# Kernel optimization log

Measured on AMD Instinct MI355X. Metric: run time of the kernel, lower is better.

Reference implementation:

```python
import jax, jax.numpy as jnp
import numpy as np

HID = 1152
MLP = 4304
NH = 16
HD = HID // NH  # 72
S = 3072
SEGS = 6
EPS = 1e-5


def setup_inputs() -> dict:
    key = jax.random.key(0)
    ks = jax.random.split(key, 16)
    sc = 0.02
    x = jax.random.normal(ks[0], (S, HID), jnp.float32)
    input_row_offsets = (jnp.arange(SEGS + 1, dtype=jnp.int32) * (S // SEGS))
    ang = jax.random.uniform(ks[1], (S, HD // 2), jnp.float32) * 6.2831853
    freqs_cis = jnp.stack([jnp.cos(ang), jnp.sin(ang)], axis=-1)  # [S,36,2]
    return {
        'x': x,
        'input_row_offsets': input_row_offsets,
        'freqs_cis': freqs_cis,
        'ln0_g': jnp.ones((HID,), jnp.float32),
        'ln0_b': jnp.zeros((HID,), jnp.float32),
        'wqkv_w': jax.random.normal(ks[2], (HID, 3 * HID), jnp.float32) * sc,
        'wqkv_b': jnp.zeros((3 * HID,), jnp.float32),
        'wo_w': jax.random.normal(ks[3], (HID, HID), jnp.float32) * sc,
        'wo_b': jnp.zeros((HID,), jnp.float32),
        'ln1_g': jnp.ones((HID,), jnp.float32),
        'ln1_b': jnp.zeros((HID,), jnp.float32),
        'mlp_w1': jax.random.normal(ks[4], (HID, MLP), jnp.float32) * sc,
        'mlp_b1': jnp.zeros((MLP,), jnp.float32),
        'mlp_w2': jax.random.normal(ks[5], (MLP, HID), jnp.float32) * sc,
        'mlp_b2': jnp.zeros((HID,), jnp.float32),
    }


def _layernorm(x, g, b):
    mu = jnp.mean(x, axis=-1, keepdims=True)
    var = jnp.mean(jnp.square(x - mu), axis=-1, keepdims=True)
    return (x - mu) * jax.lax.rsqrt(var + EPS) * g + b


def _rope(x, fc):
    # x: [S, H, D]; fc: [S, D//2, 2] (cos, sin). Complex multiply on (even, odd) pairs.
    s, h, d = x.shape
    xr = x.reshape(s, h, d // 2, 2)
    a, b = xr[..., 0], xr[..., 1]
    c = fc[:, None, :, 0]
    sn = fc[:, None, :, 1]
    return jnp.stack([a * c - b * sn, a * sn + b * c], axis=-1).reshape(s, h, d)


def _block(x, input_row_offsets, freqs_cis, ln0_g, ln0_b, wqkv_w, wqkv_b,
           wo_w, wo_b, ln1_g, ln1_b, mlp_w1, mlp_b1, mlp_w2, mlp_b2):
    s = x.shape[0]
    residual = x
    h = _layernorm(x, ln0_g, ln0_b)
    qkv = (h @ wqkv_w + wqkv_b).reshape(s, 3, NH, HD)
    xq, xk, xv = qkv[:, 0], qkv[:, 1], qkv[:, 2]  # [S,H,D]
    xq = _rope(xq, freqs_cis)
    xk = _rope(xk, freqs_cis)
    # Block-diagonal mask from row offsets; NOTE: original adds bool mask as 0/1.
    tok = jnp.arange(s)
    seg = jnp.searchsorted(input_row_offsets, tok, side='right') - 1
    mask = (seg[:, None] == seg[None, :]).astype(xq.dtype)  # [S,S]
    scores = jnp.einsum('shd,thd->hst', xq, xk) / np.sqrt(HD) + mask[None]
    attn = jax.nn.softmax(scores.astype(jnp.float32), axis=-1).astype(xq.dtype)
    out = jnp.einsum('hst,thd->shd', attn, xv).reshape(s, HID)
    x = residual + (out @ wo_w + wo_b)
    residual = x
    h = _layernorm(x, ln1_g, ln1_b)
    h = jax.nn.gelu(h @ mlp_w1 + mlp_b1, approximate=True) @ mlp_w2 + mlp_b2
    return residual + h


def reference(x, input_row_offsets, freqs_cis, ln0_g, ln0_b, wqkv_w, wqkv_b,
              wo_w, wo_b, ln1_g, ln1_b, mlp_w1, mlp_b1, mlp_w2, mlp_b2):
    return _block(x, input_row_offsets, freqs_cis, ln0_g, ln0_b, wqkv_w,
                  wqkv_b, wo_w, wo_b, ln1_g, ln1_b, mlp_w1, mlp_b1, mlp_w2,
                  mlp_b2)
```

## Files before the change

### kernel.cpp

```cpp
#include <hip/hip_runtime.h>
#include <hip/hip_bf16.h>
#include <cstddef>

#define S_TOT 3072
#define HID_  1152
#define MLP_  4304
#define MLPP_ 4352
#define NH_   16
#define HD_   72
#define SEGS_ 6
#define EPS_  1e-5f

typedef __attribute__((ext_vector_type(8))) short short8;
typedef __attribute__((ext_vector_type(4))) float floatx4;
typedef unsigned short ushort;
typedef unsigned int uint;

__device__ __forceinline__ ushort f2bf(float x)
{
    __hip_bfloat16 h = __float2bfloat16(x);
    return *reinterpret_cast<ushort*>(&h);
}
__device__ __forceinline__ float bf2f(ushort u)
{
    __hip_bfloat16 h = *reinterpret_cast<__hip_bfloat16*>(&u);
    return __bfloat162float(h);
}

__device__ __forceinline__ float gelu_tanh(float x)
{
    float x3 = x * x * x;
    return 0.5f * x * (1.0f + tanhf(0.7978845608028654f * (x + 0.044715f * x3)));
}

__device__ __forceinline__ float bperm_f(int srclane, float v)
{
    return __int_as_float(__builtin_amdgcn_ds_bpermute(srclane * 4, __float_as_int(v)));
}

__global__ __launch_bounds__(256)
void ln_bf_kernel(const float* __restrict__ x, const float* __restrict__ g,
                  const float* __restrict__ b, ushort* __restrict__ yh,
                  ushort* __restrict__ yl)
{
    int row  = blockIdx.x * 4 + (threadIdx.x >> 6);
    int lane = threadIdx.x & 63;
    const float* xr = x + (size_t)row * HID_;
    float v[18];
    float s = 0.f;
#pragma unroll
    for (int i = 0; i < 18; ++i) { v[i] = xr[lane + i * 64]; s += v[i]; }
#pragma unroll
    for (int o = 32; o; o >>= 1) s += __shfl_xor(s, o);
    float mu = s * (1.0f / (float)HID_);
    float vs = 0.f;
#pragma unroll
    for (int i = 0; i < 18; ++i) { float d = v[i] - mu; vs += d * d; }
#pragma unroll
    for (int o = 32; o; o >>= 1) vs += __shfl_xor(vs, o);
    float rstd = rsqrtf(vs * (1.0f / (float)HID_) + EPS_);
#pragma unroll
    for (int i = 0; i < 18; ++i) {
        int c = lane + i * 64;
        float val = (v[i] - mu) * rstd * g[c] + b[c];
        ushort hi = f2bf(val);
        yh[(size_t)row * HID_ + c] = hi;
        yl[(size_t)row * HID_ + c] = f2bf(val - bf2f(hi));
    }
}

__global__ __launch_bounds__(256)
void convt_kernel(const float* __restrict__ in, ushort* __restrict__ oh,
                  ushort* __restrict__ ol, int Kin, int Nin, int Kout)
{
    __shared__ float t[32][33];
    int n0 = blockIdx.x * 32, k0 = blockIdx.y * 32;
    int tx = threadIdx.x & 31, ty = threadIdx.x >> 5;
#pragma unroll
    for (int j = 0; j < 4; ++j) {
        int k = k0 + ty + 8 * j, n = n0 + tx;
        t[ty + 8 * j][tx] = (k < Kin && n < Nin) ? in[(size_t)k * Nin + n] : 0.f;
    }
    __syncthreads();
#pragma unroll
    for (int j = 0; j < 4; ++j) {
        int n = n0 + ty + 8 * j, k = k0 + tx;
        float v = t[tx][ty + 8 * j];
        ushort hi = f2bf(v);
        oh[(size_t)n * Kout + k] = hi;
        if (ol) ol[(size_t)n * Kout + k] = f2bf(v - bf2f(hi));
    }
}

__device__ __forceinline__ int swz(int row, int ke)
{
    return (row * 32 + ke) ^ ((row & 7) << 3);
}

template<int ACT, bool HAS_RES, bool OUT_PAIR>
__global__ __launch_bounds__(256)
void gemm_bf16x2_kernel(const ushort* __restrict__ Ah, const ushort* __restrict__ Al,
                        const ushort* __restrict__ Bh,
                        const float* __restrict__ bias, const float* __restrict__ res,
                        float* __restrict__ C, ushort* __restrict__ Chi,
                        ushort* __restrict__ Clo, int M, int N, int K, int Ns)
{
    __shared__ ushort sAh[128 * 32], sAl[128 * 32], sBh[128 * 32];

    const int tid = threadIdx.x;
    const int bm = blockIdx.y * 128, bn = blockIdx.x * 128;
    const int lane = tid & 63, wv = tid >> 6;
    const int lm = lane & 15, lg = lane >> 4;
    const int wr = wv >> 1, wc = wv & 1;

    const int srow = tid >> 2, skb = (tid & 3) * 8;
    const size_t aoff0 = (size_t)(bm + srow) * K + skb;
    const size_t aoff1 = (size_t)(bm + srow + 64) * K + skb;
    const size_t boff0 = (size_t)(bn + srow) * K + skb;
    const size_t boff1 = (size_t)(bn + srow + 64) * K + skb;

    short8 rAh0, rAh1, rAl0, rAl1, rBh0, rBh1;
    auto LOAD = [&](int k0) {
        rAh0 = *reinterpret_cast<const short8*>(Ah + aoff0 + k0);
        rAh1 = *reinterpret_cast<const short8*>(Ah + aoff1 + k0);
        rAl0 = *reinterpret_cast<const short8*>(Al + aoff0 + k0);
        rAl1 = *reinterpret_cast<const short8*>(Al + aoff1 + k0);
        rBh0 = *reinterpret_cast<const short8*>(Bh + boff0 + k0);
        rBh1 = *reinterpret_cast<const short8*>(Bh + boff1 + k0);
    };

    floatx4 acc[4][4] = {};
    LOAD(0);

    const int w0 = swz(srow, skb), w1 = swz(srow + 64, skb);
    for (int k0 = 0; k0 < K; k0 += 32) {
        *reinterpret_cast<short8*>(&sAh[w0]) = rAh0;
        *reinterpret_cast<short8*>(&sAh[w1]) = rAh1;
        *reinterpret_cast<short8*>(&sAl[w0]) = rAl0;
        *reinterpret_cast<short8*>(&sAl[w1]) = rAl1;
        *reinterpret_cast<short8*>(&sBh[w0]) = rBh0;
        *reinterpret_cast<short8*>(&sBh[w1]) = rBh1;
        __syncthreads();
        if (k0 + 32 < K) LOAD(k0 + 32);

        short8 bhf[4];
#pragma unroll
        for (int j = 0; j < 4; ++j) {
            int o = swz(wc * 64 + j * 16 + lm, 8 * lg);
            bhf[j] = *reinterpret_cast<const short8*>(&sBh[o]);
        }
#pragma unroll
        for (int i = 0; i < 4; ++i) {
            int o = swz(wr * 64 + i * 16 + lm, 8 * lg);
            short8 ahf = *reinterpret_cast<const short8*>(&sAh[o]);
            short8 alf = *reinterpret_cast<const short8*>(&sAl[o]);
#pragma unroll
            for (int j = 0; j < 4; ++j) {
                acc[i][j] = __builtin_amdgcn_mfma_f32_16x16x32_bf16(ahf, bhf[j], acc[i][j], 0, 0, 0);
                acc[i][j] = __builtin_amdgcn_mfma_f32_16x16x32_bf16(alf, bhf[j], acc[i][j], 0, 0, 0);
            }
        }
        __syncthreads();
    }

#pragma unroll
    for (int i = 0; i < 4; ++i) {
#pragma unroll
        for (int j = 0; j < 4; ++j) {
#pragma unroll
            for (int r = 0; r < 4; ++r) {
                int m = bm + wr * 64 + i * 16 + lg * 4 + r;
                int n = bn + wc * 64 + j * 16 + lm;
                if (OUT_PAIR) {
                    float v = 0.f;
                    if (n < N) {
                        v = acc[i][j][r] + bias[n];
                        if (ACT == 1) v = gelu_tanh(v);
                    }
                    ushort hi = f2bf(v);
                    Chi[(size_t)m * Ns + n] = hi;
                    Clo[(size_t)m * Ns + n] = f2bf(v - bf2f(hi));
                } else if (n < N) {
                    float v = acc[i][j][r] + bias[n];
                    if (ACT == 1) v = gelu_tanh(v);
                    if (HAS_RES) v += res[(size_t)m * Ns + n];
                    C[(size_t)m * Ns + n] = v;
                }
            }
        }
    }
}

__global__ __launch_bounds__(256)
void qkv_post_kernel(const float* __restrict__ qkv, const float* __restrict__ fc,
                     ushort* __restrict__ qh, ushort* __restrict__ kh,
                     ushort* __restrict__ vt)
{
    const int t0 = blockIdx.x * 64, head = blockIdx.y, tid = threadIdx.x;
    const float kscale = 0.11785113019775793f;
#pragma unroll
    for (int p = 0; p < 2; ++p) {
        ushort* dst = p ? kh : qh;
        float sc = p ? 1.0f : kscale;
        for (int c = tid; c < 64 * 36; c += 256) {
            int t = c / 36, j = c % 36;
            size_t src = (size_t)(t0 + t) * (3 * HID_) + (size_t)p * HID_ + head * HD_ + 2 * j;
            float a = qkv[src], b = qkv[src + 1];
            float cs = fc[(size_t)(t0 + t) * HD_ + 2 * j];
            float sn = fc[(size_t)(t0 + t) * HD_ + 2 * j + 1];
            float o0 = (a * cs - b * sn) * sc, o1 = (a * sn + b * cs) * sc;
            uint u = (uint)f2bf(o0) | ((uint)f2bf(o1) << 16);
            *reinterpret_cast<uint*>(&dst[((size_t)head * S_TOT + t0 + t) * 96 + 2 * j]) = u;
        }
        for (int c = tid; c < 64 * 12; c += 256) {
            int t = c / 12, q = c % 12;
            *reinterpret_cast<uint*>(&dst[((size_t)head * S_TOT + t0 + t) * 96 + 72 + 2 * q]) = 0u;
        }
    }
    __shared__ ushort vs[72][76];
    for (int c = tid; c < 64 * 72; c += 256) {
        int t = c / 72, d = c % 72;
        vs[d][t] = f2bf(qkv[(size_t)(t0 + t) * (3 * HID_) + 2 * HID_ + head * HD_ + d]);
    }
    __syncthreads();
    for (int c = tid; c < 80 * 16; c += 256) {
        int d = c / 16, ch = c % 16;
        uint lo = 0, hi = 0;
        if (d < HD_) {
            lo = (uint)vs[d][ch * 4]     | ((uint)vs[d][ch * 4 + 1] << 16);
            hi = (uint)vs[d][ch * 4 + 2] | ((uint)vs[d][ch * 4 + 3] << 16);
        }
        uint2 u; u.x = lo; u.y = hi;
        *reinterpret_cast<uint2*>(&vt[((size_t)head * 80 + d) * S_TOT + t0 + ch * 4]) = u;
    }
}

#define QBLK 64
#define KVBLK 64
#define KSS 104
#define VTS2 104
#define PLS 72

__global__ __launch_bounds__(256)
void attn_mfma3_kernel(const ushort* __restrict__ qh, const ushort* __restrict__ kh,
                       const ushort* __restrict__ vt, const int* __restrict__ offs,
                       ushort* __restrict__ oh, ushort* __restrict__ ol)
{
    __shared__ alignas(16) ushort Ks[KVBLK * KSS];
    __shared__ alignas(16) ushort Vt[80 * VTS2];
    __shared__ alignas(16) ushort Pl[QBLK * PLS];

    const int qt   = blockIdx.x;
    const int head = blockIdx.y;
    const int tid  = threadIdx.x;
    const int lane = tid & 63;
    const int wv   = tid >> 6;
    const int lm   = lane & 15;
    const int lg   = lane >> 4;
    const int q0   = qt * QBLK;

    int ofv[SEGS_ + 1];
#pragma unroll
    for (int i = 0; i <= SEGS_; ++i) ofv[i] = offs[i];
    auto segof = [&](int t) {
        int s = 0;
#pragma unroll
        for (int i = 1; i <= SEGS_; ++i) s += (t >= ofv[i]);
        return s;
    };

    short8 qf[3];
#pragma unroll
    for (int ks = 0; ks < 3; ++ks)
        qf[ks] = *reinterpret_cast<const short8*>(
            &qh[((size_t)head * S_TOT + q0 + wv * 16 + lm) * 96 + ks * 32 + 8 * lg]);

    const int qseg = segof(q0 + wv * 16 + lm);

    floatx4 of[5] = {};
    float m_run = -1e30f, l_run = 0.f;

    for (int kt = 0; kt < S_TOT / KVBLK; ++kt) {
        const int kv0 = kt * KVBLK;
#pragma unroll
        for (int k = 0; k < 3; ++k) {
            int c = tid + k * 256;
            int r = c / 12, off = (c % 12) * 8;
            *reinterpret_cast<short8*>(&Ks[r * KSS + off]) =
                *reinterpret_cast<const short8*>(&kh[((size_t)head * S_TOT + kv0 + r) * 96 + off]);
        }
#pragma unroll
        for (int k = 0; k < 3; ++k) {
            int c = tid + k * 256;
            if (c < 640) {
                int r = c / 8, off = (c % 8) * 8;
                *reinterpret_cast<short8*>(&Vt[r * VTS2 + off]) =
                    *reinterpret_cast<const short8*>(&vt[((size_t)head * 80 + r) * S_TOT + kv0 + off]);
            }
        }
        __syncthreads();

        floatx4 sf[4];
#pragma unroll
        for (int ct = 0; ct < 4; ++ct) {
            floatx4 acc = {0.f, 0.f, 0.f, 0.f};
#pragma unroll
            for (int ks = 0; ks < 3; ++ks) {
                short8 kb = *reinterpret_cast<const short8*>(
                    &Ks[(ct * 16 + lm) * KSS + ks * 32 + 8 * lg]);
                acc = __builtin_amdgcn_mfma_f32_16x16x32_bf16(kb, qf[ks], acc, 0, 0, 0);
            }
            sf[ct] = acc;
        }

        int ks0 = segof(kv0), ks1 = segof(kv0 + KVBLK - 1);
        float b = 0.f;
        if (ks0 == ks1) {
            b = (qseg == ks0) ? 1.0f : 0.0f;
        } else {
#pragma unroll
            for (int ct = 0; ct < 4; ++ct)
#pragma unroll
                for (int r = 0; r < 4; ++r) {
                    int ksg = segof(kv0 + 16 * ct + 4 * lg + r);
                    sf[ct][r] += (qseg == ksg) ? 1.0f : 0.0f;
                }
        }

        float mx = fmaxf(fmaxf(fmaxf(sf[0][0], sf[0][1]), fmaxf(sf[0][2], sf[0][3])),
                         fmaxf(fmaxf(sf[1][0], sf[1][1]), fmaxf(sf[1][2], sf[1][3])));
        mx = fmaxf(mx, fmaxf(fmaxf(fmaxf(sf[2][0], sf[2][1]), fmaxf(sf[2][2], sf[2][3])),
                             fmaxf(fmaxf(sf[3][0], sf[3][1]), fmaxf(sf[3][2], sf[3][3]))));
        mx = fmaxf(mx, __shfl_xor(mx, 16));
        mx = fmaxf(mx, __shfl_xor(mx, 32));
        float mt = mx + b;

        if (__any((int)(mt > m_run))) {
            float mn = fmaxf(m_run, mt);
            float s = __expf(m_run - mn);
            m_run = mn;
            l_run *= s;
            float s_r[4];
#pragma unroll
            for (int r = 0; r < 4; ++r) s_r[r] = bperm_f(4 * lg + r, s);
#pragma unroll
            for (int ct = 0; ct < 5; ++ct)
#pragma unroll
                for (int r = 0; r < 4; ++r) of[ct][r] *= s_r[r];
        }

        float c = m_run - b;
        float sum = 0.f;
#pragma unroll
        for (int ct = 0; ct < 4; ++ct)
#pragma unroll
            for (int r = 0; r < 4; ++r) {
                float p = __expf(sf[ct][r] - c);
                sf[ct][r] = p;
                sum += p;
            }
        sum += __shfl_xor(sum, 16);
        sum += __shfl_xor(sum, 32);
        l_run += sum;

#pragma unroll
        for (int ct = 0; ct < 4; ++ct) {
            uint w0 = (uint)f2bf(sf[ct][0]) | ((uint)f2bf(sf[ct][1]) << 16);
            uint w1 = (uint)f2bf(sf[ct][2]) | ((uint)f2bf(sf[ct][3]) << 16);
            int e = (wv * 16 + lm) * PLS + 16 * ct + 4 * lg;
            *reinterpret_cast<uint*>(&Pl[e])     = w0;
            *reinterpret_cast<uint*>(&Pl[e + 2]) = w1;
        }

        short8 pa0 = *reinterpret_cast<const short8*>(&Pl[(wv * 16 + lm) * PLS + 8 * lg]);
        short8 pa1 = *reinterpret_cast<const short8*>(&Pl[(wv * 16 + lm) * PLS + 32 + 8 * lg]);

#pragma unroll
        for (int ct = 0; ct < 5; ++ct) {
            short8 v0 = *reinterpret_cast<const short8*>(&Vt[(ct * 16 + lm) * VTS2 + 8 * lg]);
            short8 v1 = *reinterpret_cast<const short8*>(&Vt[(ct * 16 + lm) * VTS2 + 32 + 8 * lg]);
            of[ct] = __builtin_amdgcn_mfma_f32_16x16x32_bf16(pa0, v0, of[ct], 0, 0, 0);
            of[ct] = __builtin_amdgcn_mfma_f32_16x16x32_bf16(pa1, v1, of[ct], 0, 0, 0);
        }
        __syncthreads();
    }

    float invl = 1.0f / l_run;
    float inv_r[4];
#pragma unroll
    for (int r = 0; r < 4; ++r) inv_r[r] = bperm_f(4 * lg + r, invl);
#pragma unroll
    for (int ct = 0; ct < 5; ++ct) {
        int d = ct * 16 + lm;
        if (d < HD_) {
#pragma unroll
            for (int r = 0; r < 4; ++r) {
                int row = q0 + wv * 16 + lg * 4 + r;
                float v = of[ct][r] * inv_r[r];
                ushort hi = f2bf(v);
                oh[(size_t)row * HID_ + head * HD_ + d] = hi;
                ol[(size_t)row * HID_ + head * HD_ + d] = f2bf(v - bf2f(hi));
            }
        }
    }
}

extern "C" void kernel_launch(void* const* d_in, const int* in_sizes, int n_in,
                              void* d_out, int out_size, void* d_ws, size_t ws_size,
                              hipStream_t stream)
{
    const float* x      = (const float*)d_in[0];
    const int*   offs   = (const int*)  d_in[1];
    const float* fc     = (const float*)d_in[2];
    const float* ln0_g  = (const float*)d_in[3];
    const float* ln0_b  = (const float*)d_in[4];
    const float* wqkv_w = (const float*)d_in[5];
    const float* wqkv_b = (const float*)d_in[6];
    const float* wo_w   = (const float*)d_in[7];
    const float* wo_b   = (const float*)d_in[8];
    const float* ln1_g  = (const float*)d_in[9];
    const float* ln1_b  = (const float*)d_in[10];
    const float* w1     = (const float*)d_in[11];
    const float* b1     = (const float*)d_in[12];
    const float* w2     = (const float*)d_in[13];
    const float* b2     = (const float*)d_in[14];
    float* outp = (float*)d_out;

    char* base = (char*)d_ws;
    const size_t SZ_X2    = (size_t)S_TOT * HID_ * 4;
    const size_t SZ_HPAIR = (size_t)S_TOT * HID_ * 2;
    const size_t SZ_W1E   = (size_t)MLPP_ * HID_ * 2;
    const size_t SZ_QKV   = (size_t)S_TOT * 3 * HID_ * 4;

    float*  x2      = (float*)(base + 0);
    float*  qkv     = (float*)(base + 0);
    ushort* h2_h    = (ushort*)(base + SZ_X2);
    ushort* h2_l    = h2_h + (size_t)S_TOT * HID_;
    ushort* woT_h   = (ushort*)(base + SZ_X2);
    ushort* w2T_h   = (ushort*)(base + SZ_X2);
    ushort* w1T_h   = (ushort*)(base + SZ_X2 + 2 * SZ_HPAIR);
    ushort* mid_h   = (ushort*)(base + SZ_X2 + 2 * SZ_HPAIR + 2 * SZ_W1E);
    ushort* mid_l   = mid_h + (size_t)S_TOT * MLPP_;
    ushort* h_h     = (ushort*)(base + SZ_QKV);
    ushort* h_l     = h_h + (size_t)S_TOT * HID_;
    ushort* aout_h  = h_h;
    ushort* aout_l  = h_l;
    ushort* wqkvT_h = (ushort*)(base + SZ_QKV + 2 * SZ_HPAIR);
    ushort* qh      = (ushort*)(base + SZ_QKV + 2 * SZ_HPAIR);
    ushort* kh      = qh + (size_t)NH_ * S_TOT * 96;
    ushort* vt      = kh + (size_t)NH_ * S_TOT * 96;

    convt_kernel<<<dim3(3456 / 32, 1152 / 32), 256, 0, stream>>>(
        wqkv_w, wqkvT_h, nullptr, 1152, 3456, 1152);
    ln_bf_kernel<<<S_TOT / 4, 256, 0, stream>>>(x, ln0_g, ln0_b, h_h, h_l);
    gemm_bf16x2_kernel<0, false, false><<<dim3(3456 / 128, S_TOT / 128), 256, 0, stream>>>(
        h_h, h_l, wqkvT_h, wqkv_b, nullptr, qkv, nullptr, nullptr,
        S_TOT, 3456, 1152, 3456);
    qkv_post_kernel<<<dim3(S_TOT / 64, NH_), 256, 0, stream>>>(qkv, fc, qh, kh, vt);
    attn_mfma3_kernel<<<dim3(S_TOT / QBLK, NH_), 256, 0, stream>>>(
        qh, kh, vt, offs, aout_h, aout_l);
    convt_kernel<<<dim3(1152 / 32, 1152 / 32), 256, 0, stream>>>(
        wo_w, woT_h, nullptr, 1152, 1152, 1152);
    gemm_bf16x2_kernel<0, true, false><<<dim3(HID_ / 128, S_TOT / 128), 256, 0, stream>>>(
        aout_h, aout_l, woT_h, wo_b, x, x2, nullptr, nullptr,
        S_TOT, HID_, 1152, HID_);
    ln_bf_kernel<<<S_TOT / 4, 256, 0, stream>>>(x2, ln1_g, ln1_b, h2_h, h2_l);
    convt_kernel<<<dim3(MLPP_ / 32, 1152 / 32), 256, 0, stream>>>(
        w1, w1T_h, nullptr, 1152, MLP_, 1152);
    gemm_bf16x2_kernel<1, false, true><<<dim3(MLPP_ / 128, S_TOT / 128), 256, 0, stream>>>(
        h2_h, h2_l, w1T_h, b1, nullptr, nullptr, mid_h, mid_l,
        S_TOT, MLP_, 1152, MLPP_);
    convt_kernel<<<dim3(1152 / 32, MLPP_ / 32), 256, 0, stream>>>(
        w2, w2T_h, nullptr, MLP_, 1152, MLPP_);
    gemm_bf16x2_kernel<0, true, false><<<dim3(HID_ / 128, S_TOT / 128), 256, 0, stream>>>(
        mid_h, mid_l, w2T_h, b2, x2, outp, nullptr, nullptr,
        S_TOT, HID_, MLPP_, HID_);
}
```

Measured before the change: 635.6 us.

## Double-buffer GEMM tiles with direct global-to-LDS loads

The bf16x2 GEMM now copies tiles straight from global memory into a double-buffered LDS tile using global_load_lds. Previously each tile went through registers and then an LDS store. This removes the register staging and one of the two barriers per k-step, so the next tile's load can overlap the MFMA work on the current one. In exchange it doubles LDS use per block and drops the XOR swizzle, so the LDS fragment reads may hit more bank conflicts.

New measurement: 652.4 us. 1.03x slower.

```diff
diff --git a/kernel.cpp b/kernel.cpp
--- a/kernel.cpp
+++ b/kernel.cpp
@@ -38,6 +38,13 @@
     return __int_as_float(__builtin_amdgcn_ds_bpermute(srclane * 4, __float_as_int(v)));
 }
 
+typedef __attribute__((address_space(3))) void lds_void_t;
+typedef __attribute__((address_space(1))) const void gconst_void_t;
+__device__ __forceinline__ void gload_lds16(const ushort* g, ushort* l)
+{
+    __builtin_amdgcn_global_load_lds((gconst_void_t*)g, (lds_void_t*)l, 16, 0, 0);
+}
+
 __global__ __launch_bounds__(256)
 void ln_bf_kernel(const float* __restrict__ x, const float* __restrict__ g,
                   const float* __restrict__ b, ushort* __restrict__ yh,
@@ -90,11 +97,6 @@
         oh[(size_t)n * Kout + k] = hi;
         if (ol) ol[(size_t)n * Kout + k] = f2bf(v - bf2f(hi));
     }
-}
-
-__device__ __forceinline__ int swz(int row, int ke)
-{
-    return (row * 32 + ke) ^ ((row & 7) << 3);
 }
 
 template<int ACT, bool HAS_RES, bool OUT_PAIR>
@@ -105,7 +107,9 @@
                         float* __restrict__ C, ushort* __restrict__ Chi,
                         ushort* __restrict__ Clo, int M, int N, int K, int Ns)
 {
-    __shared__ ushort sAh[128 * 32], sAl[128 * 32], sBh[128 * 32];
+    __shared__ ushort sAh[2][128 * 32];
+    __shared__ ushort sAl[2][128 * 32];
+    __shared__ ushort sBh[2][128 * 32];
 
     const int tid = threadIdx.x;
     const int bm = blockIdx.y * 128, bn = blockIdx.x * 128;
@@ -113,54 +117,45 @@
     const int lm = lane & 15, lg = lane >> 4;
     const int wr = wv >> 1, wc = wv & 1;
 
-    const int srow = tid >> 2, skb = (tid & 3) * 8;
-    const size_t aoff0 = (size_t)(bm + srow) * K + skb;
-    const size_t aoff1 = (size_t)(bm + srow + 64) * K + skb;
-    const size_t boff0 = (size_t)(bn + srow) * K + skb;
-    const size_t boff1 = (size_t)(bn + srow + 64) * K + skb;
-
-    short8 rAh0, rAh1, rAl0, rAl1, rBh0, rBh1;
-    auto LOAD = [&](int k0) {
-        rAh0 = *reinterpret_cast<const short8*>(Ah + aoff0 + k0);
-        rAh1 = *reinterpret_cast<const short8*>(Ah + aoff1 + k0);
-        rAl0 = *reinterpret_cast<const short8*>(Al + aoff0 + k0);
-        rAl1 = *reinterpret_cast<const short8*>(Al + aoff1 + k0);
-        rBh0 = *reinterpret_cast<const short8*>(Bh + boff0 + k0);
-        rBh1 = *reinterpret_cast<const short8*>(Bh + boff1 + k0);
+    const int l4 = lane >> 2, kb8 = (lane & 3) * 8;
+    const size_t ga0 = (size_t)(bm + 32 * wv + l4) * K + kb8;
+    const size_t ga1 = ga0 + (size_t)16 * K;
+    const size_t gb0 = (size_t)(bn + 32 * wv + l4) * K + kb8;
+    const size_t gb1 = gb0 + (size_t)16 * K;
+    const int la = wv * 1024;
+
+    auto ISSUE = [&](int k0, int b) {
+        gload_lds16(Ah + ga0 + k0, &sAh[b][la]);
+        gload_lds16(Ah + ga1 + k0, &sAh[b][la + 512]);
+        gload_lds16(Al + ga0 + k0, &sAl[b][la]);
+        gload_lds16(Al + ga1 + k0, &sAl[b][la + 512]);
+        gload_lds16(Bh + gb0 + k0, &sBh[b][la]);
+        gload_lds16(Bh + gb1 + k0, &sBh[b][la + 512]);
     };
 
     floatx4 acc[4][4] = {};
-    LOAD(0);
-
-    const int w0 = swz(srow, skb), w1 = swz(srow + 64, skb);
-    for (int k0 = 0; k0 < K; k0 += 32) {
-        *reinterpret_cast<short8*>(&sAh[w0]) = rAh0;
-        *reinterpret_cast<short8*>(&sAh[w1]) = rAh1;
-        *reinterpret_cast<short8*>(&sAl[w0]) = rAl0;
-        *reinterpret_cast<short8*>(&sAl[w1]) = rAl1;
-        *reinterpret_cast<short8*>(&sBh[w0]) = rBh0;
-        *reinterpret_cast<short8*>(&sBh[w1]) = rBh1;
+    ISSUE(0, 0);
+    const int nt = K / 32;
+    for (int t = 0; t < nt; ++t) {
         __syncthreads();
-        if (k0 + 32 < K) LOAD(k0 + 32);
-
+        if (t + 1 < nt) ISSUE((t + 1) * 32, (t + 1) & 1);
+        const int b = t & 1;
         short8 bhf[4];
 #pragma unroll
-        for (int j = 0; j < 4; ++j) {
-            int o = swz(wc * 64 + j * 16 + lm, 8 * lg);
-            bhf[j] = *reinterpret_cast<const short8*>(&sBh[o]);
-        }
+        for (int j = 0; j < 4; ++j)
+            bhf[j] = *reinterpret_cast<const short8*>(
+                &sBh[b][(wc * 64 + j * 16 + lm) * 32 + 8 * lg]);
 #pragma unroll
         for (int i = 0; i < 4; ++i) {
-            int o = swz(wr * 64 + i * 16 + lm, 8 * lg);
-            short8 ahf = *reinterpret_cast<const short8*>(&sAh[o]);
-            short8 alf = *reinterpret_cast<const short8*>(&sAl[o]);
+            int ro = (wr * 64 + i * 16 + lm) * 32 + 8 * lg;
+            short8 ahf = *reinterpret_cast<const short8*>(&sAh[b][ro]);
+            short8 alf = *reinterpret_cast<const short8*>(&sAl[b][ro]);
 #pragma unroll
             for (int j = 0; j < 4; ++j) {
                 acc[i][j] = __builtin_amdgcn_mfma_f32_16x16x32_bf16(ahf, bhf[j], acc[i][j], 0, 0, 0);
                 acc[i][j] = __builtin_amdgcn_mfma_f32_16x16x32_bf16(alf, bhf[j], acc[i][j], 0, 0, 0);
             }
         }
-        __syncthreads();
     }
 
 #pragma unroll
```
